# Kernel optimization log

Hardware: AMD Instinct MI355X
Metric: run time of the kernel (lower is better)

The kernel has to match this reference:

```python
import jax, jax.numpy as jnp
import numpy as np

B, C_IN, C_HID, H, W = 4, 512, 512, 64, 64


def setup_inputs() -> dict:
    key = jax.random.key(0)
    ks = jax.random.split(key, 9)
    s_in = 1.0 / np.sqrt(C_IN)
    s_hid = 1.0 / np.sqrt(C_HID)
    return {
        "inp": jax.random.normal(ks[0], (B, C_IN, H, W), dtype=jnp.float32),
        "Wk": jax.random.normal(ks[1], (C_HID, C_IN), dtype=jnp.float32) * s_in,
        "bk": jax.random.normal(ks[2], (C_HID,), dtype=jnp.float32) * 0.01,
        "Wq": jax.random.normal(ks[3], (C_HID, C_IN), dtype=jnp.float32) * s_in,
        "bq": jax.random.normal(ks[4], (C_HID,), dtype=jnp.float32) * 0.01,
        "Wv": jax.random.normal(ks[5], (C_HID, C_IN), dtype=jnp.float32) * s_in,
        "bv": jax.random.normal(ks[6], (C_HID,), dtype=jnp.float32) * 0.01,
        "Wo": jax.random.normal(ks[7], (C_IN, C_HID), dtype=jnp.float32) * s_hid,
        "bo": jax.random.normal(ks[8], (C_IN,), dtype=jnp.float32) * 0.01,
    }


def reference(inp, Wk, bk, Wq, bq, Wv, bv, Wo, bo):
    b, _, h, w = inp.shape
    n = h * w

    def conv1x1(x, Wt, bias):  # 1x1 conv == per-pixel GEMM
        return jnp.einsum('bchw,oc->bohw', x, Wt) + bias[None, :, None, None]

    k = conv1x1(inp, Wk, bk).reshape(b, C_HID, n)   # [B,Ch,N]
    q = conv1x1(inp, Wq, bq).reshape(b, C_HID, n)
    v = conv1x1(inp, Wv, bv).reshape(b, C_HID, n)

    scale = 1.0 / jnp.sqrt(jnp.asarray(C_HID, dtype=jnp.float32))
    # weight[b,i,j] = <key_i, query_j> / sqrt(Ch); softmax over j (dim=2)
    scores = jnp.einsum('bci,bcj->bij', k, q) * scale  # [B,N,N]
    weight = jax.nn.softmax(scores, axis=2)
    # out[b,c,i] = sum_j weight[b,i,j] * v[b,c,j]
    out = jnp.einsum('bij,bcj->bci', weight, v).reshape(b, C_HID, h, w)
    return conv1x1(out, Wo, bo)  # [B,C_in,H,W]
```

## Files before the change

### kernel.cpp

```cpp
#include <hip/hip_runtime.h>
#include <hip/hip_bf16.h>


typedef __attribute__((ext_vector_type(4))) float f32x4;
typedef __attribute__((ext_vector_type(8))) short short8;
typedef __attribute__((ext_vector_type(4))) short short4v;

#define QSCALE 0.06376639774f
#define FENCE asm volatile("" ::: "memory")
#define SBAR  __builtin_amdgcn_s_barrier()

__device__ __forceinline__ unsigned short f2bf(float f) {
  unsigned u = __builtin_bit_cast(unsigned, f);
  unsigned r = (u + 0x7FFFu + ((u >> 16) & 1u)) >> 16;
  return (unsigned short)r;
}

__device__ __forceinline__ void gll16(const void* g, void* l) {
  __builtin_amdgcn_global_load_lds((const __attribute__((address_space(1))) void*)g,
                                   (__attribute__((address_space(3))) void*)l, 16, 0, 0);
}

#define MFMA_BF16(d, va, vb) \
  d = __builtin_amdgcn_mfma_f32_16x16x32_bf16(va, vb, d, 0, 0, 0)

__device__ __forceinline__ void gemm256_core(
    const short* __restrict__ A, int lda,
    const short* __restrict__ B, int ldb,
    int nkt, char* sm, f32x4 (&acc)[8][4]) {
  const int tid = threadIdx.x, w = tid >> 6, lane = tid & 63;
  const int g = lane >> 4, l15 = lane & 15;
  const int wm = w >> 2, wn = w & 3;
  const int swz = (l15 & 7) << 4;
  const int brow = (wn & 1) << 6;

  auto stageA = [&](int buf, int h, int kt) {
    char* dst = sm + (((buf << 1) | h) << 14) + (w << 10);
    const char* gs = (const char*)A + ((size_t)(h * 128) * lda + (size_t)kt * 64) * 2;
#pragma unroll
    for (int q = 0; q < 2; ++q) {
      int o = (q << 13) | (w << 10) | (lane << 4);
      int row = o >> 7, cb = (o & 127) ^ ((row & 7) << 4);
      gll16(gs + (size_t)row * (lda * 2) + cb, dst + (q << 13));
    }
  };
  auto stageB = [&](int buf, int h, int kt) {
    char* dst = sm + 65536 + (((buf << 1) | h) << 14) + (w << 10);
    const char* gs = (const char*)B + ((size_t)(h * 128) * ldb + (size_t)kt * 64) * 2;
#pragma unroll
    for (int q = 0; q < 2; ++q) {
      int o = (q << 13) | (w << 10) | (lane << 4);
      int row = o >> 7, cb = (o & 127) ^ ((row & 7) << 4);
      gll16(gs + (size_t)row * (ldb * 2) + cb, dst + (q << 13));
    }
  };

  stageA(0, 0, 0); stageA(0, 1, 0); stageB(0, 0, 0); stageB(0, 1, 0);
  stageA(1, 0, 1); stageA(1, 1, 1); stageB(1, 0, 1); stageB(1, 1, 1);
  asm volatile("s_waitcnt vmcnt(8)" ::: "memory");
  SBAR; FENCE;

  for (int t = 0; t < nkt; ++t) {
    const int buf = t & 1;
    const char* SA = sm + (((buf << 1) | wm) << 14);
    const char* SB = sm + 65536 + (((buf << 1) | (wn >> 1)) << 14);
    short8 a[8][2], b[4][2];
#pragma unroll
    for (int mf = 0; mf < 8; ++mf)
      a[mf][0] = *(const short8*)(SA + (mf * 16 + l15) * 128 + ((g * 16) ^ swz));
#pragma unroll
    for (int nf = 0; nf < 4; ++nf)
      b[nf][0] = *(const short8*)(SB + (brow + nf * 16 + l15) * 128 + ((g * 16) ^ swz));
#pragma unroll
    for (int mf = 0; mf < 8; ++mf)
      a[mf][1] = *(const short8*)(SA + (mf * 16 + l15) * 128 + ((64 + g * 16) ^ swz));
#pragma unroll
    for (int nf = 0; nf < 4; ++nf)
      b[nf][1] = *(const short8*)(SB + (brow + nf * 16 + l15) * 128 + ((64 + g * 16) ^ swz));
    __builtin_amdgcn_s_setprio(1);
#pragma unroll
    for (int mf = 0; mf < 4; ++mf)
#pragma unroll
      for (int nf = 0; nf < 4; ++nf)
        MFMA_BF16(acc[mf][nf], a[mf][0], b[nf][0]);
    __builtin_amdgcn_s_setprio(0);
    asm volatile("s_waitcnt lgkmcnt(0)" ::: "memory");
    SBAR; FENCE;
    if (t + 2 < nkt) { stageA(buf, 0, t + 2); stageA(buf, 1, t + 2); }
    __builtin_amdgcn_s_setprio(1);
#pragma unroll
    for (int mf = 4; mf < 8; ++mf)
#pragma unroll
      for (int nf = 0; nf < 4; ++nf)
        MFMA_BF16(acc[mf][nf], a[mf][0], b[nf][0]);
    __builtin_amdgcn_s_setprio(0);
    if (t + 2 < nkt) { stageB(buf, 0, t + 2); stageB(buf, 1, t + 2); }
    __builtin_amdgcn_s_setprio(1);
#pragma unroll
    for (int mf = 0; mf < 4; ++mf)
#pragma unroll
      for (int nf = 0; nf < 4; ++nf)
        MFMA_BF16(acc[mf][nf], a[mf][1], b[nf][1]);
#pragma unroll
    for (int mf = 4; mf < 8; ++mf)
#pragma unroll
      for (int nf = 0; nf < 4; ++nf)
        MFMA_BF16(acc[mf][nf], a[mf][1], b[nf][1]);
    __builtin_amdgcn_s_setprio(0);
    if (t + 2 < nkt)      asm volatile("s_waitcnt vmcnt(8)" ::: "memory");
    else if (t + 1 < nkt) asm volatile("s_waitcnt vmcnt(0)" ::: "memory");
    SBAR; FENCE;
  }
}

#define BOUNCE256_WRITE(smp, row, colb, val) \
  *(short*)((smp) + (row) * 512 + (((colb)) ^ (((row) & 7) << 4))) = (val)

__device__ __forceinline__ void bounce256_flush(const char* smp, short* gbase,
                                                int pitch ) {
  const int tid = threadIdx.x;
  SBAR; FENCE;
#pragma unroll
  for (int it = 0; it < 16; ++it) {
    int row = (tid >> 5) + it * 16;
    short8 v = *(const short8*)(smp + row * 512 + (((tid & 31) * 16) ^ ((row & 7) << 4)));
    *(short8*)(gbase + (size_t)row * pitch + (tid & 31) * 8) = v;
  }
}

__device__ __forceinline__ void gemm_core(const short* __restrict__ A, int lda,
                                          const short* __restrict__ B, int ldb,
                                          int nk, short* lds, f32x4 (&acc)[4][4]) {
  const int tid = threadIdx.x, w = tid >> 6, lane = tid & 63;
  const int g = lane >> 4, l15 = lane & 15;
  const int wr = w >> 1, wc = w & 1;
  const int rsub = lane >> 2, slot = lane & 3;
  char* la = (char*)lds;
  char* lb = (char*)(lds + 128 * 32);
  for (int ki = 0; ki < nk; ++ki) {
    const int k0 = ki * 32;
    __syncthreads();
#pragma unroll
    for (int q = 0; q < 2; ++q) {
      int qq = w * 2 + q;
      int row = qq * 16 + rsub;
      int soff = ((slot ^ (row & 3)) * 16);
      gll16((const char*)(A + (size_t)row * lda + k0) + soff, la + qq * 1024);
      gll16((const char*)(B + (size_t)row * ldb + k0) + soff, lb + qq * 1024);
    }
    __syncthreads();
    short8 am[4], bn[4];
#pragma unroll
    for (int m = 0; m < 4; ++m) {
      int row = wr * 64 + m * 16 + l15;
      am[m] = *(const short8*)(la + row * 64 + ((g * 16) ^ ((l15 & 3) << 4)));
    }
#pragma unroll
    for (int n = 0; n < 4; ++n) {
      int row = wc * 64 + n * 16 + l15;
      bn[n] = *(const short8*)(lb + row * 64 + ((g * 16) ^ ((l15 & 3) << 4)));
    }
#pragma unroll
    for (int m = 0; m < 4; ++m)
#pragma unroll
      for (int n = 0; n < 4; ++n)
        MFMA_BF16(acc[m][n], am[m], bn[n]);
  }
}

#define BOUNCE_WRITE(lds2, row, col, val) \
  (lds2)[(row) * 128 + ((col) ^ (((row) & 7) << 3))] = (val)

#define BOUNCE_FLUSH(lds2, gbase, pitch)                                        \
  do {                                                                          \
    __syncthreads();                                                            \
    _Pragma("unroll")                                                           \
    for (int it_ = 0; it_ < 8; ++it_) {                                         \
      int row_ = (threadIdx.x >> 4) + it_ * 16;                                 \
      short8 v_ = *(const short8*)&(lds2)[row_ * 128 +                          \
                      (((threadIdx.x & 15) * 8) ^ ((row_ & 7) << 3))];          \
      *(short8*)((gbase) + (size_t)row_ * (pitch) + (threadIdx.x & 15) * 8) = v_;\
    }                                                                           \
  } while (0)

__global__ __launch_bounds__(256) void cvt_w_kernel(
    const float* __restrict__ wk, const float* __restrict__ wq,
    const float* __restrict__ wv, const float* __restrict__ wo,
    short* __restrict__ o) {
  int z = blockIdx.y;
  const float* s = (z == 0) ? wk : (z == 1) ? wq : (z == 2) ? wv : wo;
  int i = blockIdx.x * 256 + threadIdx.x;
  float4 f = ((const float4*)s)[i];
  short4v v;
  v[0] = (short)f2bf(f.x); v[1] = (short)f2bf(f.y);
  v[2] = (short)f2bf(f.z); v[3] = (short)f2bf(f.w);
  if (z < 3) {
    *(short4v*)(o + z * 262144 + i * 4) = v;
  } else {
    int idx = i * 4, co = idx >> 9, cc = idx & 511;
    short* base = o + 786432 + co * 1024 + cc;
    *(short4v*)base = v;
    *(short4v*)(base + 512) = v;
  }
}

__global__ __launch_bounds__(256) void transpose_x_kernel(
    const float* __restrict__ inp, short* __restrict__ xt) {
  __shared__ float t[32][33];
  int tx = threadIdx.x, ty = threadIdx.y;
  int n0 = blockIdx.x * 32, c0 = blockIdx.y * 32, b = blockIdx.z;
  const float* src = inp + ((size_t)(b * 512 + c0)) * 4096 + n0;
#pragma unroll
  for (int r = 0; r < 4; ++r) t[ty + r * 8][tx] = src[(ty + r * 8) * 4096 + tx];
  __syncthreads();
  short* dst = xt + ((size_t)((b << 12) + n0)) * 512 + c0;
#pragma unroll
  for (int r = 0; r < 4; ++r) dst[(ty + r * 8) * 512 + tx] = (short)f2bf(t[tx][ty + r * 8]);
}

__global__ __launch_bounds__(256) void gemm_kqv_kernel(
    const short* __restrict__ xt,
    const short* __restrict__ wk, const short* __restrict__ wq, const short* __restrict__ wv,
    const float* __restrict__ bk, const float* __restrict__ bq, const float* __restrict__ bv,
    short* __restrict__ kt, short* __restrict__ qt, short* __restrict__ vc) {
  const int z = blockIdx.z;
  __shared__ char smk[32768];
  short* lds = (short*)smk;
  short* lds2 = (short*)smk;
  const short *A, *B;
  int arow0, brow0;
  if (z < 2) { arow0 = blockIdx.x * 128; brow0 = blockIdx.y * 128;
               A = xt + (size_t)arow0 * 512; B = ((z == 0) ? wk : wq) + (size_t)brow0 * 512; }
  else       { arow0 = blockIdx.y * 128; brow0 = blockIdx.x * 128;
               A = wv + (size_t)arow0 * 512; B = xt + (size_t)brow0 * 512; }
  f32x4 acc[4][4] = {};
  gemm_core(A, 512, B, 512, 16, lds, acc);
  const int tid = threadIdx.x, w = tid >> 6, lane = tid & 63;
  const int g = lane >> 4, l15 = lane & 15;
  const int wr = w >> 1, wc = w & 1;
  __syncthreads();
#pragma unroll
  for (int m = 0; m < 4; ++m)
#pragma unroll
    for (int n = 0; n < 4; ++n)
#pragma unroll
      for (int r = 0; r < 4; ++r) {
        int row = wr * 64 + m * 16 + g * 4 + r, col = wc * 64 + n * 16 + l15;
        float v = acc[m][n][r], val;
        if (z == 0)      val = (v + bk[brow0 + col]) * QSCALE;
        else if (z == 1) val = v + bq[brow0 + col];
        else             val = v + bv[arow0 + row];
        BOUNCE_WRITE(lds2, row, col, (short)f2bf(val));
      }
  short* gbase; int pitch;
  if (z == 0)      { gbase = kt + (size_t)arow0 * 512 + brow0; pitch = 512; }
  else if (z == 1) { gbase = qt + (size_t)arow0 * 512 + brow0; pitch = 512; }
  else             { gbase = vc + (size_t)arow0 * 16384 + brow0; pitch = 16384; }
  BOUNCE_FLUSH(lds2, gbase, pitch);
}

__global__ __launch_bounds__(512, 2) void gemm_s256_kernel(
    const short* __restrict__ kt, const short* __restrict__ qt,
    short* __restrict__ P, float* __restrict__ Lpart) {
  extern __shared__ char sm[];
  const int b = blockIdx.z & 3, h = blockIdx.z >> 2;
  const int i0 = blockIdx.y * 256, jt0 = blockIdx.x * 256;
  const short* A = kt + ((size_t)(b << 12) + i0) * 512;
  const short* B = qt + ((size_t)((b << 12) + h * 2048 + jt0)) * 512;
  f32x4 acc[8][4] = {};
  gemm256_core(A, 512, B, 512, 8, sm, acc);
  const int tid = threadIdx.x, w = tid >> 6, lane = tid & 63;
  const int g = lane >> 4, l15 = lane & 15;
  const int wm = w >> 2, wn = w & 3;
  const int jp = (h * 2048 + jt0 + wn * 64) >> 6;
  float* Lp = Lpart + (((size_t)b * 64 + jp) << 12) + i0 + wm * 128;
#pragma unroll
  for (int mf = 0; mf < 8; ++mf) {
    float psum[4] = {0.f, 0.f, 0.f, 0.f};
#pragma unroll
    for (int nf = 0; nf < 4; ++nf)
#pragma unroll
      for (int r = 0; r < 4; ++r) {
        float p = exp2f(acc[mf][nf][r]);
        psum[r] += p;
        int row = wm * 128 + mf * 16 + g * 4 + r;
        int colb = (wn * 64 + nf * 16 + l15) * 2;
        BOUNCE256_WRITE(sm, row, colb, (short)f2bf(p));
      }
#pragma unroll
    for (int r = 0; r < 4; ++r) {
      float s = psum[r];
      s += __shfl_xor(s, 1); s += __shfl_xor(s, 2);
      s += __shfl_xor(s, 4); s += __shfl_xor(s, 8);
      if (l15 == 0) Lp[mf * 16 + g * 4 + r] = s;
    }
  }
  short* gbase = P + (size_t)h * 33554432 + ((size_t)((b << 12) + i0)) * 2048 + jt0;
  bounce256_flush(sm, gbase, 2048);
}

__global__ __launch_bounds__(512, 2) void gemm_pv256_kernel(
    const short* __restrict__ P, const short* __restrict__ vc,
    short* __restrict__ otab) {
  extern __shared__ char sm[];
  const int b = blockIdx.z & 3, h = blockIdx.z >> 2;
  const int i0 = blockIdx.y * 256, c0 = blockIdx.x * 256;
  const short* A = P + (size_t)h * 33554432 + ((size_t)((b << 12) + i0)) * 2048;
  const short* B = vc + (size_t)c0 * 16384 + (b << 12) + h * 2048;
  f32x4 acc[8][4] = {};
  gemm256_core(A, 2048, B, 16384, 32, sm, acc);
  const int tid = threadIdx.x, w = tid >> 6, lane = tid & 63;
  const int g = lane >> 4, l15 = lane & 15;
  const int wm = w >> 2, wn = w & 3;
#pragma unroll
  for (int mf = 0; mf < 8; ++mf)
#pragma unroll
    for (int nf = 0; nf < 4; ++nf)
#pragma unroll
      for (int r = 0; r < 4; ++r) {
        int row = wm * 128 + mf * 16 + g * 4 + r;
        int colb = (wn * 64 + nf * 16 + l15) * 2;
        BOUNCE256_WRITE(sm, row, colb, (short)f2bf(acc[mf][nf][r]));
      }
  short* gbase = otab + ((size_t)((b << 12) + i0)) * 1024 + h * 512 + c0;
  bounce256_flush(sm, gbase, 1024);
}

__global__ __launch_bounds__(256) void lred_kernel(
    const float* __restrict__ Lpart, float* __restrict__ linv) {
  int i = blockIdx.x * 256 + threadIdx.x;
  int b = i >> 12;
  float s = 0.f;
#pragma unroll 8
  for (int jp = 0; jp < 64; ++jp) s += Lpart[(((size_t)b * 64 + jp) << 12) + (i & 4095)];
  linv[i] = 1.0f / s;
}

__global__ __launch_bounds__(256) void gemm_out_kernel(
    const short* __restrict__ wdup, const short* __restrict__ otab,
    const float* __restrict__ bo, const float* __restrict__ linv,
    float* __restrict__ out) {
  __shared__ short lds[2 * 128 * 32];
  const int b = blockIdx.z;
  const int arow0 = blockIdx.y * 128;
  const int bn0 = blockIdx.x * 128;
  const short* A = wdup + (size_t)arow0 * 1024;
  const short* B = otab + ((size_t)((b << 12) + bn0)) * 1024;
  f32x4 acc[4][4] = {};
  gemm_core(A, 1024, B, 1024, 32, lds, acc);
  const int tid = threadIdx.x, w = tid >> 6, lane = tid & 63;
  const int g = lane >> 4, l15 = lane & 15;
  const int wr = w >> 1, wc = w & 1;
#pragma unroll
  for (int m = 0; m < 4; ++m) {
    int co = arow0 + wr * 64 + m * 16 + g * 4;
#pragma unroll
    for (int n = 0; n < 4; ++n) {
      int nl = bn0 + wc * 64 + n * 16 + l15;
      float li = linv[(b << 12) + nl];
#pragma unroll
      for (int r = 0; r < 4; ++r)
        out[((size_t)(b * 512 + co + r) << 12) + nl] = acc[m][n][r] * li + bo[co + r];
    }
  }
}

extern "C" void kernel_launch(void* const* d_in, const int* in_sizes, int n_in,
                              void* d_out, int out_size, void* d_ws, size_t ws_size,
                              hipStream_t stream) {
  const float* inp = (const float*)d_in[0];
  const float* Wk = (const float*)d_in[1];
  const float* bk = (const float*)d_in[2];
  const float* Wq = (const float*)d_in[3];
  const float* bq = (const float*)d_in[4];
  const float* Wv = (const float*)d_in[5];
  const float* bv = (const float*)d_in[6];
  const float* Wo = (const float*)d_in[7];
  const float* bo = (const float*)d_in[8];
  float* out = (float*)d_out;
  char* ws = (char*)d_ws;
  const size_t MB = 1048576;
  short* kt    = (short*)(ws);
  short* qt    = (short*)(ws + 16 * MB);
  short* vc    = (short*)(ws + 32 * MB);
  short* wb    = (short*)(ws + 48 * MB);
  short* xt    = (short*)(ws + 51 * MB);
  float* Lpart = (float*)(ws + 51 * MB);
  float* linv  = (float*)(ws + 55 * MB);
  short* P     = (short*)(ws + 67 * MB);
  short* otab  = (short*)(ws + 195 * MB);

  (void)in_sizes; (void)n_in; (void)out_size; (void)ws_size;

  hipFuncSetAttribute((const void*)gemm_s256_kernel,
                      hipFuncAttributeMaxDynamicSharedMemorySize, 131072);
  hipFuncSetAttribute((const void*)gemm_pv256_kernel,
                      hipFuncAttributeMaxDynamicSharedMemorySize, 131072);

  cvt_w_kernel<<<dim3(256, 4), 256, 0, stream>>>(Wk, Wq, Wv, Wo, wb);
  transpose_x_kernel<<<dim3(128, 16, 4), dim3(32, 8, 1), 0, stream>>>(inp, xt);
  gemm_kqv_kernel<<<dim3(128, 4, 3), 256, 0, stream>>>(
      xt, wb, wb + 262144, wb + 524288, bk, bq, bv, kt, qt, vc);
  gemm_s256_kernel<<<dim3(8, 16, 8), 512, 131072, stream>>>(kt, qt, P, Lpart);
  gemm_pv256_kernel<<<dim3(2, 16, 8), 512, 131072, stream>>>(P, vc, otab);
  lred_kernel<<<64, 256, 0, stream>>>(Lpart, linv);
  gemm_out_kernel<<<dim3(32, 4, 4), 256, 0, stream>>>(wb + 786432, otab, bo, linv, out);
}
```

Measured before the change: 274.8 us.

## Use 256-tile GEMM for KQV projection and remap block IDs for XCD locality

```diff
diff --git a/kernel.cpp b/kernel.cpp
--- a/kernel.cpp
+++ b/kernel.cpp
@@ -167,21 +167,6 @@
         MFMA_BF16(acc[m][n], am[m], bn[n]);
   }
 }
-
-#define BOUNCE_WRITE(lds2, row, col, val) \
-  (lds2)[(row) * 128 + ((col) ^ (((row) & 7) << 3))] = (val)
-
-#define BOUNCE_FLUSH(lds2, gbase, pitch)                                        \
-  do {                                                                          \
-    __syncthreads();                                                            \
-    _Pragma("unroll")                                                           \
-    for (int it_ = 0; it_ < 8; ++it_) {                                         \
-      int row_ = (threadIdx.x >> 4) + it_ * 16;                                 \
-      short8 v_ = *(const short8*)&(lds2)[row_ * 128 +                          \
-                      (((threadIdx.x & 15) * 8) ^ ((row_ & 7) << 3))];          \
-      *(short8*)((gbase) + (size_t)row_ * (pitch) + (threadIdx.x & 15) * 8) = v_;\
-    }                                                                           \
-  } while (0)
 
 __global__ __launch_bounds__(256) void cvt_w_kernel(
     const float* __restrict__ wk, const float* __restrict__ wq,
@@ -218,59 +203,68 @@
   for (int r = 0; r < 4; ++r) dst[(ty + r * 8) * 512 + tx] = (short)f2bf(t[tx][ty + r * 8]);
 }
 
-__global__ __launch_bounds__(256) void gemm_kqv_kernel(
+__global__ __launch_bounds__(512, 2) void kqv256_kernel(
     const short* __restrict__ xt,
     const short* __restrict__ wk, const short* __restrict__ wq, const short* __restrict__ wv,
     const float* __restrict__ bk, const float* __restrict__ bq, const float* __restrict__ bv,
     short* __restrict__ kt, short* __restrict__ qt, short* __restrict__ vc) {
-  const int z = blockIdx.z;
-  __shared__ char smk[32768];
-  short* lds = (short*)smk;
-  short* lds2 = (short*)smk;
+  extern __shared__ char sm[];
+  const int bid = blockIdx.x;
+  const int xcd = bid & 7, s = bid >> 3;
+  const int pg = s / 6, t = s % 6;
+  const int panel = pg * 8 + xcd;
+  const int z = (t < 4) ? (t >> 1) : 2;
   const short *A, *B;
   int arow0, brow0;
-  if (z < 2) { arow0 = blockIdx.x * 128; brow0 = blockIdx.y * 128;
-               A = xt + (size_t)arow0 * 512; B = ((z == 0) ? wk : wq) + (size_t)brow0 * 512; }
-  else       { arow0 = blockIdx.y * 128; brow0 = blockIdx.x * 128;
-               A = wv + (size_t)arow0 * 512; B = xt + (size_t)brow0 * 512; }
-  f32x4 acc[4][4] = {};
-  gemm_core(A, 512, B, 512, 16, lds, acc);
-  const int tid = threadIdx.x, w = tid >> 6, lane = tid & 63;
-  const int g = lane >> 4, l15 = lane & 15;
-  const int wr = w >> 1, wc = w & 1;
-  __syncthreads();
-#pragma unroll
-  for (int m = 0; m < 4; ++m)
-#pragma unroll
-    for (int n = 0; n < 4; ++n)
+  if (z < 2) {
+    arow0 = panel * 256; brow0 = (t & 1) * 256;
+    A = xt + (size_t)arow0 * 512;
+    B = ((z == 0) ? wk : wq) + (size_t)brow0 * 512;
+  } else {
+    arow0 = (t - 4) * 256; brow0 = panel * 256;
+    A = wv + (size_t)arow0 * 512;
+    B = xt + (size_t)brow0 * 512;
+  }
+  f32x4 acc[8][4] = {};
+  gemm256_core(A, 512, B, 512, 8, sm, acc);
+  const int tid = threadIdx.x, w = tid >> 6, lane = tid & 63;
+  const int gq = lane >> 4, l15 = lane & 15;
+  const int wm = w >> 2, wn = w & 3;
+#pragma unroll
+  for (int mf = 0; mf < 8; ++mf)
+#pragma unroll
+    for (int nf = 0; nf < 4; ++nf)
 #pragma unroll
       for (int r = 0; r < 4; ++r) {
-        int row = wr * 64 + m * 16 + g * 4 + r, col = wc * 64 + n * 16 + l15;
-        float v = acc[m][n][r], val;
+        int row = wm * 128 + mf * 16 + gq * 4 + r;
+        int col = wn * 64 + nf * 16 + l15;
+        float v = acc[mf][nf][r], val;
         if (z == 0)      val = (v + bk[brow0 + col]) * QSCALE;
         else if (z == 1) val = v + bq[brow0 + col];
         else             val = v + bv[arow0 + row];
-        BOUNCE_WRITE(lds2, row, col, (short)f2bf(val));
+        BOUNCE256_WRITE(sm, row, col * 2, (short)f2bf(val));
       }
   short* gbase; int pitch;
   if (z == 0)      { gbase = kt + (size_t)arow0 * 512 + brow0; pitch = 512; }
   else if (z == 1) { gbase = qt + (size_t)arow0 * 512 + brow0; pitch = 512; }
   else             { gbase = vc + (size_t)arow0 * 16384 + brow0; pitch = 16384; }
-  BOUNCE_FLUSH(lds2, gbase, pitch);
+  bounce256_flush(sm, gbase, pitch);
 }
 
 __global__ __launch_bounds__(512, 2) void gemm_s256_kernel(
     const short* __restrict__ kt, const short* __restrict__ qt,
     short* __restrict__ P, float* __restrict__ Lpart) {
   extern __shared__ char sm[];
-  const int b = blockIdx.z & 3, h = blockIdx.z >> 2;
-  const int i0 = blockIdx.y * 256, jt0 = blockIdx.x * 256;
+  const int bid = blockIdx.x;
+  const int xcd = bid & 7, s = bid >> 3;
+  const int b = xcd >> 1, h = xcd & 1;
+  const int jt0 = (s & 7) * 256, i0 = (s >> 3) * 256;
   const short* A = kt + ((size_t)(b << 12) + i0) * 512;
   const short* B = qt + ((size_t)((b << 12) + h * 2048 + jt0)) * 512;
   f32x4 acc[8][4] = {};
   gemm256_core(A, 512, B, 512, 8, sm, acc);
   const int tid = threadIdx.x, w = tid >> 6, lane = tid & 63;
-  const int g = lane >> 4, l15 = lane & 15;
+  const int gq = lane >> 4, l15 = lane & 15;
   const int wm = w >> 2, wn = w & 3;
   const int jp = (h * 2048 + jt0 + wn * 64) >> 6;
   float* Lp = Lpart + (((size_t)b * 64 + jp) << 12) + i0 + wm * 128;
@@ -283,16 +277,16 @@
       for (int r = 0; r < 4; ++r) {
         float p = exp2f(acc[mf][nf][r]);
         psum[r] += p;
-        int row = wm * 128 + mf * 16 + g * 4 + r;
+        int row = wm * 128 + mf * 16 + gq * 4 + r;
         int colb = (wn * 64 + nf * 16 + l15) * 2;
         BOUNCE256_WRITE(sm, row, colb, (short)f2bf(p));
       }
 #pragma unroll
     for (int r = 0; r < 4; ++r) {
-      float s = psum[r];
-      s += __shfl_xor(s, 1); s += __shfl_xor(s, 2);
-      s += __shfl_xor(s, 4); s += __shfl_xor(s, 8);
-      if (l15 == 0) Lp[mf * 16 + g * 4 + r] = s;
+      float ss = psum[r];
+      ss += __shfl_xor(ss, 1); ss += __shfl_xor(ss, 2);
+      ss += __shfl_xor(ss, 4); ss += __shfl_xor(ss, 8);
+      if (l15 == 0) Lp[mf * 16 + gq * 4 + r] = ss;
     }
   }
   short* gbase = P + (size_t)h * 33554432 + ((size_t)((b << 12) + i0)) * 2048 + jt0;
@@ -303,14 +297,16 @@
     const short* __restrict__ P, const short* __restrict__ vc,
     short* __restrict__ otab) {
   extern __shared__ char sm[];
-  const int b = blockIdx.z & 3, h = blockIdx.z >> 2;
-  const int i0 = blockIdx.y * 256, c0 = blockIdx.x * 256;
+  const int bid = blockIdx.x;
+  const int xcd = bid & 7, s = bid >> 3;
+  const int b = xcd >> 1, h = xcd & 1;
+  const int c0 = (s & 1) * 256, i0 = (s >> 1) * 256;
   const short* A = P + (size_t)h * 33554432 + ((size_t)((b << 12) + i0)) * 2048;
   const short* B = vc + (size_t)c0 * 16384 + (b << 12) + h * 2048;
   f32x4 acc[8][4] = {};
   gemm256_core(A, 2048, B, 16384, 32, sm, acc);
   const int tid = threadIdx.x, w = tid >> 6, lane = tid & 63;
-  const int g = lane >> 4, l15 = lane & 15;
+  const int gq = lane >> 4, l15 = lane & 15;
   const int wm = w >> 2, wn = w & 3;
 #pragma unroll
   for (int mf = 0; mf < 8; ++mf)
@@ -318,7 +314,7 @@
     for (int nf = 0; nf < 4; ++nf)
 #pragma unroll
       for (int r = 0; r < 4; ++r) {
-        int row = wm * 128 + mf * 16 + g * 4 + r;
+        int row = wm * 128 + mf * 16 + gq * 4 + r;
         int colb = (wn * 64 + nf * 16 + l15) * 2;
         BOUNCE256_WRITE(sm, row, colb, (short)f2bf(acc[mf][nf][r]));
       }
@@ -341,9 +337,13 @@
     const float* __restrict__ bo, const float* __restrict__ linv,
     float* __restrict__ out) {
   __shared__ short lds[2 * 128 * 32];
-  const int b = blockIdx.z;
-  const int arow0 = blockIdx.y * 128;
-  const int bn0 = blockIdx.x * 128;
+  const int bid = blockIdx.x;
+  const int xcd = bid & 7, s = bid >> 3;
+  const int cot = s & 3;
+  const int p = (s >> 2) * 8 + xcd;
+  const int nt = p & 31, b = p >> 5;
+  const int arow0 = cot * 128;
+  const int bn0 = nt * 128;
   const short* A = wdup + (size_t)arow0 * 1024;
   const short* B = otab + ((size_t)((b << 12) + bn0)) * 1024;
   f32x4 acc[4][4] = {};
@@ -392,6 +392,8 @@
 
   (void)in_sizes; (void)n_in; (void)out_size; (void)ws_size;
 
+  hipFuncSetAttribute((const void*)kqv256_kernel,
+                      hipFuncAttributeMaxDynamicSharedMemorySize, 131072);
   hipFuncSetAttribute((const void*)gemm_s256_kernel,
                       hipFuncAttributeMaxDynamicSharedMemorySize, 131072);
   hipFuncSetAttribute((const void*)gemm_pv256_kernel,
@@ -399,10 +401,10 @@
 
   cvt_w_kernel<<<dim3(256, 4), 256, 0, stream>>>(Wk, Wq, Wv, Wo, wb);
   transpose_x_kernel<<<dim3(128, 16, 4), dim3(32, 8, 1), 0, stream>>>(inp, xt);
-  gemm_kqv_kernel<<<dim3(128, 4, 3), 256, 0, stream>>>(
+  kqv256_kernel<<<384, 512, 131072, stream>>>(
       xt, wb, wb + 262144, wb + 524288, bk, bq, bv, kt, qt, vc);
-  gemm_s256_kernel<<<dim3(8, 16, 8), 512, 131072, stream>>>(kt, qt, P, Lpart);
-  gemm_pv256_kernel<<<dim3(2, 16, 8), 512, 131072, stream>>>(P, vc, otab);
+  gemm_s256_kernel<<<1024, 512, 131072, stream>>>(kt, qt, P, Lpart);
+  gemm_pv256_kernel<<<256, 512, 131072, stream>>>(P, vc, otab);
   lred_kernel<<<64, 256, 0, stream>>>(Lpart, linv);
-  gemm_out_kernel<<<dim3(32, 4, 4), 256, 0, stream>>>(wb + 786432, otab, bo, linv, out);
-}
+  gemm_out_kernel<<<512, 256, 0, stream>>>(wb + 786432, otab, bo, linv, out);
+}
```

Result: no change. 273.4 us (-0.5%).
